# Optimization experiments

Hardware: AMD Instinct MI355X
Metric: run time of the kernel (lower is better)

Reference implementation:

```python
import jax, jax.numpy as jnp
import numpy as np

N = 50000      # nodes
E = 800000     # edges (avg degree 16)
IN = 256       # in_dim == heads*hidden (so DGL residual is Identity)
H = 4          # heads
D = 64         # hidden_dim / out_dim per head
EPS = 1e-5
NEG_SLOPE_ATTN = 0.2   # DGL GATConv edge-attention leaky_relu slope
NEG_SLOPE_ACT = 0.01   # F.leaky_relu default


def gat_conv(x, src, dst, W, al, ar, b, act):
    # x: [N, H*D], W: [H*D, H*D], al/ar: [H, D], b: [H*D]
    feat = (x @ W).reshape(N, H, D)                       # [N,H,D]
    el = jnp.sum(feat * al, axis=-1)                      # [N,H]
    er = jnp.sum(feat * ar, axis=-1)                      # [N,H]
    e = jax.nn.leaky_relu(el[src] + er[dst], NEG_SLOPE_ATTN)  # [E,H]
    # segment softmax over incoming edges per destination node
    m = jax.ops.segment_max(e, dst, num_segments=N)       # [N,H]
    m = jnp.where(jnp.isfinite(m), m, 0.0)                # nodes with no in-edges
    ee = jnp.exp(e - m[dst])                              # [E,H]
    denom = jax.ops.segment_sum(ee, dst, num_segments=N)  # [N,H]
    alpha = ee / jnp.maximum(denom[dst], 1e-9)            # [E,H]
    msg = feat[src] * alpha[:, :, None]                   # [E,H,D]
    rst = jax.ops.segment_sum(msg, dst, num_segments=N)   # [N,H,D]
    rst = rst + x.reshape(N, H, D)                        # identity residual (dims match)
    rst = rst + b.reshape(1, H, D)
    if act:
        rst = jax.nn.leaky_relu(rst, NEG_SLOPE_ACT)
    return rst


def batch_norm(h, gamma, beta):
    # BatchNorm1d in training mode: batch statistics over node dim
    mu = jnp.mean(h, axis=0)
    var = jnp.var(h, axis=0)
    return (h - mu) * jax.lax.rsqrt(var + EPS) * gamma + beta


def setup_inputs():
    key = jax.random.key(0)
    ks = jax.random.split(key, 18)
    s = 1.0 / np.sqrt(IN)
    inp = {
        'x': jax.random.normal(ks[0], (N, IN), jnp.float32),
        'src': jax.random.randint(ks[1], (E,), 0, N),
        'dst': jax.random.randint(ks[2], (E,), 0, N),
    }
    names = ['W1', 'al1', 'ar1', 'b1', 'W2', 'al2', 'ar2', 'b2', 'W3', 'al3', 'ar3', 'b3']
    shapes = [(IN, H * D), (H, D), (H, D), (H * D,)] * 3
    for i, (nm, sh) in enumerate(zip(names, shapes)):
        inp[nm] = jax.random.normal(ks[3 + i], sh, jnp.float32) * s
    inp['g1'] = jnp.ones((H * D,), jnp.float32)
    inp['be1'] = jnp.zeros((H * D,), jnp.float32)
    inp['g2'] = jnp.ones((H * D,), jnp.float32)
    inp['be2'] = jnp.zeros((H * D,), jnp.float32)
    return inp


def reference(x, src, dst, W1, al1, ar1, b1, W2, al2, ar2, b2, W3, al3, ar3, b3, g1, be1, g2, be2):
    h = gat_conv(x, src, dst, W1, al1, ar1, b1, act=True).reshape(N, H * D)
    h = batch_norm(h, g1, be1)
    h = gat_conv(h, src, dst, W2, al2, ar2, b2, act=True).reshape(N, H * D)
    h = batch_norm(h, g2, be2)
    h = gat_conv(h, src, dst, W3, al3, ar3, b3, act=False)   # [N,H,D]
    return h.mean(axis=1)                                    # [N,D]
```

## Files before the change

### kernel.cpp

```cpp
#include <hip/hip_runtime.h>

constexpr int NN = 50000;
constexpr int NE = 800000;
constexpr float SLOPE_A = 0.2f;
constexpr float SLOPE_R = 0.01f;
constexpr int SCB = 196;

typedef __attribute__((ext_vector_type(8))) short bf16x8;
typedef __attribute__((ext_vector_type(4))) float f32x4;

__device__ __forceinline__ unsigned short f2bf(float f) {
    union { float f; unsigned u; } v; v.f = f;
    unsigned u = v.u;
    unsigned r = u + 0x7fffu + ((u >> 16) & 1u);
    return (unsigned short)(r >> 16);
}
__device__ __forceinline__ float bf2f(unsigned short s) {
    union { unsigned u; float f; } v; v.u = ((unsigned)s) << 16;
    return v.f;
}

__global__ void k_hist(const int* __restrict__ dst, int* __restrict__ cnt) {
    int i = blockIdx.x * 256 + threadIdx.x;
    if (i < NE) atomicAdd(&cnt[dst[i]], 1);
}

__global__ void k_scan1(const int* __restrict__ cnt, int* __restrict__ loc,
                        int* __restrict__ bsum) {
    __shared__ int sh[256];
    int t = threadIdx.x;
    int i = blockIdx.x * 256 + t;
    int v = (i < NN) ? cnt[i] : 0;
    sh[t] = v;
    __syncthreads();
    for (int off = 1; off < 256; off <<= 1) {
        int tmp = (t >= off) ? sh[t - off] : 0;
        __syncthreads();
        sh[t] += tmp;
        __syncthreads();
    }
    loc[i] = sh[t] - v;
    if (t == 255) bsum[blockIdx.x] = sh[255];
}

__global__ void k_scan2(const int* __restrict__ bsum, int* __restrict__ boff,
                        int* __restrict__ rowptr) {
    __shared__ int sh[256];
    int t = threadIdx.x;
    int v = (t < SCB) ? bsum[t] : 0;
    sh[t] = v;
    __syncthreads();
    for (int off = 1; off < 256; off <<= 1) {
        int tmp = (t >= off) ? sh[t - off] : 0;
        __syncthreads();
        sh[t] += tmp;
        __syncthreads();
    }
    if (t < SCB) boff[t] = sh[t] - v;
    if (t == 255) rowptr[NN] = sh[255];
}

__global__ void k_scan3(const int* __restrict__ loc, const int* __restrict__ boff,
                        int* __restrict__ rowptr, int* __restrict__ cursor) {
    int i = blockIdx.x * 256 + threadIdx.x;
    if (i < NN) {
        int r = loc[i] + boff[blockIdx.x];
        rowptr[i] = r;
        cursor[i] = r;
    }
}

__global__ void k_scatter(const int* __restrict__ src, const int* __restrict__ dst,
                          int* __restrict__ cursor, int* __restrict__ ssrc) {
    int i = blockIdx.x * 256 + threadIdx.x;
    if (i < NE) {
        int d = dst[i];
        int pos = atomicAdd(&cursor[d], 1);
        ssrc[pos] = src[i];
    }
}

__global__ void k_fold(const float* __restrict__ W, const float* __restrict__ sc,
                       const float* __restrict__ sh, const float* __restrict__ al,
                       const float* __restrict__ ar, unsigned short* __restrict__ Wfrag,
                       float* __restrict__ cvec, unsigned short* __restrict__ wlrfrag,
                       float* __restrict__ offlr, int has_bn) {
    int b = blockIdx.x;
    if (b < 32) {
        int gid = b * 256 + threadIdx.x;
        int lane = gid & 63;
        int frag = gid >> 6;
        int j = frag & 3, kc = (frag >> 2) & 7, w = frag >> 5;
        int mm = lane & 15, q = lane >> 4;
        int n = 64 * w + 16 * j + mm;
        int k0 = kc * 32 + q * 8;
        unsigned short o[8];
#pragma unroll
        for (int t = 0; t < 8; t++) {
            float wv = W[(size_t)(k0 + t) * 256 + n];
            if (sc) wv *= sc[k0 + t];
            o[t] = f2bf(wv);
        }
        *(uint4*)(Wfrag + (size_t)gid * 8) = *(const uint4*)o;
    } else if (has_bn && b < 288) {
        __shared__ float red[256];
        int n = b - 32, k = threadIdx.x;
        red[k] = sh[k] * W[(size_t)k * 256 + n];
        __syncthreads();
        for (int off = 128; off > 0; off >>= 1) {
            if (k < off) red[k] += red[k + off];
            __syncthreads();
        }
        if (k == 0) cvec[n] = red[0];
    } else {
        int n = b - (has_bn ? 288 : 32);
        int h = n >> 1;
        const float* a = (n & 1) ? ar : al;
        int k = threadIdx.x;
        float raw = 0.f;
#pragma unroll 8
        for (int d = 0; d < 64; d++)
            raw += W[(size_t)k * 256 + 64 * h + d] * a[h * 64 + d];
        float val = (sc ? sc[k] : 1.f) * raw;
        int kc = k >> 5, rem = k & 31, q = rem >> 3, t = rem & 7;
        wlrfrag[kc * 512 + (q * 16 + n) * 8 + t] = f2bf(val);
        wlrfrag[kc * 512 + (q * 16 + n + 8) * 8 + t] = 0;
        __shared__ float red[256];
        red[k] = sh ? sh[k] * raw : 0.f;
        __syncthreads();
        for (int off = 128; off > 0; off >>= 1) {
            if (k < off) red[k] += red[k + off];
            __syncthreads();
        }
        if (k == 0) offlr[n] = red[0];
    }
}

__launch_bounds__(256)
__global__ void k_gemm(const void* __restrict__ Araw, int af32,
                       const unsigned short* __restrict__ Wfrag,
                       const float* __restrict__ cvec,
                       const unsigned short* __restrict__ wlrfrag,
                       const float* __restrict__ offlr,
                       unsigned short* __restrict__ feat16, float* __restrict__ el,
                       float* __restrict__ er) {
    constexpr int AP = 264;
    __shared__ __align__(16) unsigned short Alds[64 * AP];
    const int tid = threadIdx.x;
    const int rowbase = blockIdx.x * 64;

    if (af32) {
        const float* A = (const float*)Araw;
        int r = tid >> 6;
        int c4 = tid & 63;
        for (int it = 0; it < 16; it++) {
            int rr = it * 4 + r;
            int gr = rowbase + rr;
            float4 v = make_float4(0.f, 0.f, 0.f, 0.f);
            if (gr < NN) v = *(const float4*)(A + (size_t)gr * 256 + c4 * 4);
            ushort4 pv;
            pv.x = f2bf(v.x); pv.y = f2bf(v.y); pv.z = f2bf(v.z); pv.w = f2bf(v.w);
            *(ushort4*)(&Alds[rr * AP + c4 * 4]) = pv;
        }
    } else {
        const unsigned short* A = (const unsigned short*)Araw;
        for (int it = 0; it < 8; it++) {
            int idx = it * 256 + tid;
            int rr = idx >> 5;
            int c16 = idx & 31;
            int gr = rowbase + rr;
            uint4 v = make_uint4(0u, 0u, 0u, 0u);
            if (gr < NN) v = *(const uint4*)(A + (size_t)gr * 256 + c16 * 8);
            *(uint4*)(&Alds[rr * AP + c16 * 8]) = v;
        }
    }
    __syncthreads();

    f32x4 acc[4][4];
    for (int i = 0; i < 4; i++)
        for (int j = 0; j < 4; j++)
            acc[i][j] = (f32x4){0.f, 0.f, 0.f, 0.f};
    f32x4 accLR[4];
    for (int i = 0; i < 4; i++) accLR[i] = (f32x4){0.f, 0.f, 0.f, 0.f};

    const int lane = tid & 63, w = tid >> 6;
    const int mm = lane & 15, q = lane >> 4;

    const unsigned short* bbase = Wfrag + ((size_t)w * 8 * 4) * 512 + (size_t)lane * 8;

#pragma unroll
    for (int kc = 0; kc < 8; kc++) {
        bf16x8 a[4], b[4];
        for (int i = 0; i < 4; i++)
            a[i] = *(const bf16x8*)(&Alds[(16 * i + mm) * AP + kc * 32 + q * 8]);
        for (int j = 0; j < 4; j++)
            b[j] = *(const bf16x8*)(bbase + (size_t)(kc * 4 + j) * 512);
        for (int i = 0; i < 4; i++)
            for (int j = 0; j < 4; j++)
                acc[i][j] = __builtin_amdgcn_mfma_f32_16x16x32_bf16(a[i], b[j], acc[i][j], 0, 0, 0);
        if (w == 0) {
            bf16x8 blr = *(const bf16x8*)(wlrfrag + kc * 512 + lane * 8);
            for (int i = 0; i < 4; i++)
                accLR[i] = __builtin_amdgcn_mfma_f32_16x16x32_bf16(a[i], blr, accLR[i], 0, 0, 0);
        }
    }
    __syncthreads();

    if (cvec) {
        float cv[4];
        for (int j = 0; j < 4; j++) cv[j] = cvec[64 * w + 16 * j + mm];
        for (int i = 0; i < 4; i++)
            for (int j = 0; j < 4; j++)
                for (int r = 0; r < 4; r++)
                    acc[i][j][r] += cv[j];
    }

    if (w == 0 && mm < 8) {
        float off = offlr[mm];
        int h = mm >> 1;
        float* dstp = (mm & 1) ? er : el;
        for (int i = 0; i < 4; i++)
            for (int r = 0; r < 4; r++) {
                int gr = rowbase + 16 * i + q * 4 + r;
                if (gr < NN) dstp[gr * 4 + h] = accLR[i][r] + off;
            }
    }

    for (int i = 0; i < 4; i++)
        for (int j = 0; j < 4; j++) {
            int gc = 64 * w + 16 * j + mm;
            for (int r = 0; r < 4; r++) {
                int rr = 16 * i + q * 4 + r;
                Alds[rr * AP + gc] = f2bf(acc[i][j][r]);
            }
        }
    __syncthreads();
    for (int it = 0; it < 8; it++) {
        int idx = it * 256 + tid;
        int rr = idx >> 5;
        int c16 = idx & 31;
        int gr = rowbase + rr;
        if (gr < NN)
            *(uint4*)(feat16 + (size_t)gr * 256 + c16 * 8) = *(const uint4*)(&Alds[rr * AP + c16 * 8]);
    }
}

__launch_bounds__(256)
__global__ void k_agg(const unsigned short* __restrict__ feat16, const float* __restrict__ el,
                      const float* __restrict__ er, const int* __restrict__ rowptr,
                      const int* __restrict__ ssrc,
                      const unsigned short* __restrict__ residh, const float* __restrict__ residf,
                      const float* __restrict__ bnscale, const float* __restrict__ bnshift,
                      int use_bn, const float* __restrict__ bias, int act,
                      unsigned short* __restrict__ outh, float* __restrict__ outf,
                      int final_mean) {
    int n = __builtin_amdgcn_readfirstlane(blockIdx.x * 4 + (threadIdx.x >> 6));
    int l = threadIdx.x & 63;
    int h = l >> 4;
    int beg = rowptr[n], end = rowptr[n + 1];
    float erh = er[n * 4 + h];

    float4 r;
    if (residf) {
        r = *(const float4*)(residf + (size_t)n * 256 + l * 4);
    } else {
        ushort4 rv = *(const ushort4*)(residh + (size_t)n * 256 + l * 4);
        r = make_float4(bf2f(rv.x), bf2f(rv.y), bf2f(rv.z), bf2f(rv.w));
    }
    float4 sc4, sh4;
    if (use_bn) {
        sc4 = *(const float4*)(bnscale + l * 4);
        sh4 = *(const float4*)(bnshift + l * 4);
    }
    float4 bb = *(const float4*)(bias + l * 4);

    float d = 0.f;
    float4 acc = make_float4(0.f, 0.f, 0.f, 0.f);

    for (int e = beg; e < end; e += 8) {
        int ss[8];
        float cc[8];
        ushort4 ff[8];
#pragma unroll
        for (int j = 0; j < 8; j++) {
            int ee = e + j;
            ss[j] = ssrc[(ee < end) ? ee : beg];
        }
#pragma unroll
        for (int j = 0; j < 8; j++)
            cc[j] = el[ss[j] * 4 + h];
#pragma unroll
        for (int j = 0; j < 8; j++)
            ff[j] = *(const ushort4*)(feat16 + (size_t)ss[j] * 256 + l * 4);
#pragma unroll
        for (int j = 0; j < 8; j++) {
            float sc = cc[j] + erh;
            sc = (sc > 0.f) ? sc : SLOPE_A * sc;
            float wgt = ((e + j) < end) ? __expf(sc) : 0.f;
            d += wgt;
            acc.x += bf2f(ff[j].x) * wgt;
            acc.y += bf2f(ff[j].y) * wgt;
            acc.z += bf2f(ff[j].z) * wgt;
            acc.w += bf2f(ff[j].w) * wgt;
        }
    }

    float invd = 1.f / fmaxf(d, 1e-9f);
    acc.x *= invd; acc.y *= invd; acc.z *= invd; acc.w *= invd;

    if (use_bn) {
        r.x = r.x * sc4.x + sh4.x;
        r.y = r.y * sc4.y + sh4.y;
        r.z = r.z * sc4.z + sh4.z;
        r.w = r.w * sc4.w + sh4.w;
    }
    acc.x += r.x + bb.x; acc.y += r.y + bb.y;
    acc.z += r.z + bb.z; acc.w += r.w + bb.w;
    if (act) {
        acc.x = (acc.x > 0.f) ? acc.x : SLOPE_R * acc.x;
        acc.y = (acc.y > 0.f) ? acc.y : SLOPE_R * acc.y;
        acc.z = (acc.z > 0.f) ? acc.z : SLOPE_R * acc.z;
        acc.w = (acc.w > 0.f) ? acc.w : SLOPE_R * acc.w;
    }

    if (!final_mean) {
        ushort4 p;
        p.x = f2bf(acc.x); p.y = f2bf(acc.y); p.z = f2bf(acc.z); p.w = f2bf(acc.w);
        *(ushort4*)(outh + (size_t)n * 256 + l * 4) = p;
    } else {
        acc.x += __shfl_xor(acc.x, 16, 64); acc.x += __shfl_xor(acc.x, 32, 64);
        acc.y += __shfl_xor(acc.y, 16, 64); acc.y += __shfl_xor(acc.y, 32, 64);
        acc.z += __shfl_xor(acc.z, 16, 64); acc.z += __shfl_xor(acc.z, 32, 64);
        acc.w += __shfl_xor(acc.w, 16, 64); acc.w += __shfl_xor(acc.w, 32, 64);
        if (l < 16) {
            acc.x *= 0.25f; acc.y *= 0.25f; acc.z *= 0.25f; acc.w *= 0.25f;
            *(float4*)(outf + (size_t)n * 64 + l * 4) = acc;
        }
    }
}

__global__ void k_bnstats(const unsigned short* __restrict__ hh, float* __restrict__ pbuf) {
    __shared__ float ps[8 * 256];
    __shared__ float ps2[8 * 256];
    int t = threadIdx.x, b = blockIdx.x;
    int r8 = t >> 5, c32 = t & 31;
    int r0 = b * 196, r1 = min(r0 + 196, NN);
    float s[8], s2[8];
#pragma unroll
    for (int e = 0; e < 8; e++) { s[e] = 0.f; s2[e] = 0.f; }
    for (int r = r0 + r8; r < r1; r += 8) {
        uint4 v = *(const uint4*)(hh + (size_t)r * 256 + c32 * 8);
        const unsigned short* pv = (const unsigned short*)&v;
#pragma unroll
        for (int e = 0; e < 8; e++) {
            float f = bf2f(pv[e]);
            s[e] += f; s2[e] += f * f;
        }
    }
#pragma unroll
    for (int e = 0; e < 8; e++) {
        ps[r8 * 256 + c32 * 8 + e] = s[e];
        ps2[r8 * 256 + c32 * 8 + e] = s2[e];
    }
    __syncthreads();
    float ts = 0.f, ts2 = 0.f;
    for (int g = 0; g < 8; g++) { ts += ps[g * 256 + t]; ts2 += ps2[g * 256 + t]; }
    pbuf[b * 512 + t] = ts;
    pbuf[b * 512 + 256 + t] = ts2;
}

__global__ void k_bnfinal(const float* __restrict__ pbuf, const float* __restrict__ g,
                          const float* __restrict__ be, float* __restrict__ scale,
                          float* __restrict__ shift) {
    int t = threadIdx.x;
    float s = 0.f, s2 = 0.f;
    for (int b = 0; b < 256; b++) {
        s += pbuf[b * 512 + t];
        s2 += pbuf[b * 512 + 256 + t];
    }
    float mu = s * (1.f / NN);
    float var = s2 * (1.f / NN) - mu * mu;
    float rs = rsqrtf(var + 1e-5f);
    float sc = rs * g[t];
    scale[t] = sc;
    shift[t] = be[t] - mu * sc;
}

extern "C" void kernel_launch(void* const* d_in, const int* in_sizes, int n_in,
                              void* d_out, int out_size, void* d_ws, size_t ws_size,
                              hipStream_t stream) {
    const float* x   = (const float*)d_in[0];
    const int* src   = (const int*)d_in[1];
    const int* dst   = (const int*)d_in[2];
    const float* W1  = (const float*)d_in[3];
    const float* al1 = (const float*)d_in[4];
    const float* ar1 = (const float*)d_in[5];
    const float* b1  = (const float*)d_in[6];
    const float* W2  = (const float*)d_in[7];
    const float* al2 = (const float*)d_in[8];
    const float* ar2 = (const float*)d_in[9];
    const float* b2  = (const float*)d_in[10];
    const float* W3  = (const float*)d_in[11];
    const float* al3 = (const float*)d_in[12];
    const float* ar3 = (const float*)d_in[13];
    const float* b3  = (const float*)d_in[14];
    const float* g1  = (const float*)d_in[15];
    const float* be1 = (const float*)d_in[16];
    const float* g2  = (const float*)d_in[17];
    const float* be2 = (const float*)d_in[18];
    float* out = (float*)d_out;

    char* ws = (char*)d_ws;
    size_t off = 0;
    auto alloc = [&](size_t bytes) {
        void* p = ws + off;
        off += (bytes + 255) & ~(size_t)255;
        return p;
    };
    int* rowptr = (int*)alloc((NN + 1) * sizeof(int));
    int* cursor = (int*)alloc(NN * sizeof(int));
    int* cnt    = (int*)alloc(SCB * 256 * sizeof(int));
    int* loc    = (int*)alloc(SCB * 256 * sizeof(int));
    int* bsum   = (int*)alloc(SCB * sizeof(int));
    int* boff   = (int*)alloc(SCB * sizeof(int));
    int* ssrc   = (int*)alloc(NE * sizeof(int));
    unsigned short* feat16 = (unsigned short*)alloc((size_t)NN * 256 * sizeof(unsigned short));
    unsigned short* hbuf   = (unsigned short*)alloc((size_t)NN * 256 * sizeof(unsigned short));
    float* el   = (float*)alloc((size_t)NN * 4 * sizeof(float));
    float* er   = (float*)alloc((size_t)NN * 4 * sizeof(float));
    unsigned short* Wfrag1  = (unsigned short*)alloc(65536 * sizeof(unsigned short));
    unsigned short* Wfrag2  = (unsigned short*)alloc(65536 * sizeof(unsigned short));
    unsigned short* wlrfrag = (unsigned short*)alloc(4096 * sizeof(unsigned short));
    float* offlr   = (float*)alloc(16 * sizeof(float));
    float* cvec    = (float*)alloc(256 * sizeof(float));
    float* pbuf    = (float*)alloc(256 * 512 * sizeof(float));
    float* bnscale = (float*)alloc(256 * sizeof(float));
    float* bnshift = (float*)alloc(256 * sizeof(float));

    hipMemsetAsync(cnt, 0, NN * sizeof(int), stream);
    k_hist<<<(NE + 255) / 256, 256, 0, stream>>>(dst, cnt);
    k_scan1<<<SCB, 256, 0, stream>>>(cnt, loc, bsum);
    k_scan2<<<1, 256, 0, stream>>>(bsum, boff, rowptr);
    k_scan3<<<SCB, 256, 0, stream>>>(loc, boff, rowptr, cursor);
    k_scatter<<<(NE + 255) / 256, 256, 0, stream>>>(src, dst, cursor, ssrc);
    k_fold<<<40, 256, 0, stream>>>(W1, nullptr, nullptr, al1, ar1,
                                   Wfrag1, nullptr, wlrfrag, offlr, 0);

    const int GB = (NN + 63) / 64;
    const int NB = NN / 4;

    k_gemm<<<GB, 256, 0, stream>>>(x, 1, Wfrag1, nullptr, wlrfrag, offlr, feat16, el, er);
    k_agg<<<NB, 256, 0, stream>>>(feat16, el, er, rowptr, ssrc, nullptr, x,
                                  nullptr, nullptr, 0, b1, 1, hbuf, nullptr, 0);
    k_bnstats<<<256, 256, 0, stream>>>(hbuf, pbuf);
    k_bnfinal<<<1, 256, 0, stream>>>(pbuf, g1, be1, bnscale, bnshift);
    k_fold<<<296, 256, 0, stream>>>(W2, bnscale, bnshift, al2, ar2,
                                    Wfrag2, cvec, wlrfrag, offlr, 1);

    k_gemm<<<GB, 256, 0, stream>>>(hbuf, 0, Wfrag2, cvec, wlrfrag, offlr, feat16, el, er);
    k_agg<<<NB, 256, 0, stream>>>(feat16, el, er, rowptr, ssrc, hbuf, nullptr,
                                  bnscale, bnshift, 1, b2, 1, hbuf, nullptr, 0);
    k_bnstats<<<256, 256, 0, stream>>>(hbuf, pbuf);
    k_bnfinal<<<1, 256, 0, stream>>>(pbuf, g2, be2, bnscale, bnshift);
    k_fold<<<296, 256, 0, stream>>>(W3, bnscale, bnshift, al3, ar3,
                                    Wfrag2, cvec, wlrfrag, offlr, 1);

    k_gemm<<<GB, 256, 0, stream>>>(hbuf, 0, Wfrag2, cvec, wlrfrag, offlr, feat16, el, er);
    k_agg<<<NB, 256, 0, stream>>>(feat16, el, er, rowptr, ssrc, hbuf, nullptr,
                                  bnscale, bnshift, 1, b3, 0, nullptr, out, 1);
}
```

Measured before the change: 550.3 us.

## Precompute per-edge attention weights and split wave into two edge halves with 16-byte gathers

```diff
diff --git a/kernel.cpp b/kernel.cpp
--- a/kernel.cpp
+++ b/kernel.cpp
@@ -18,6 +18,12 @@
 __device__ __forceinline__ float bf2f(unsigned short s) {
     union { unsigned u; float f; } v; v.u = ((unsigned)s) << 16;
     return v.f;
+}
+__device__ __forceinline__ float bflo(unsigned u) {
+    union { unsigned u; float f; } v; v.u = u << 16; return v.f;
+}
+__device__ __forceinline__ float bfhi(unsigned u) {
+    union { unsigned u; float f; } v; v.u = u & 0xffff0000u; return v.f;
 }
 
 __global__ void k_hist(const int* __restrict__ dst, int* __restrict__ cnt) {
@@ -71,12 +77,14 @@
 }
 
 __global__ void k_scatter(const int* __restrict__ src, const int* __restrict__ dst,
-                          int* __restrict__ cursor, int* __restrict__ ssrc) {
+                          int* __restrict__ cursor, int* __restrict__ ssrc,
+                          int* __restrict__ sdst) {
     int i = blockIdx.x * 256 + threadIdx.x;
     if (i < NE) {
         int d = dst[i];
         int pos = atomicAdd(&cursor[d], 1);
         ssrc[pos] = src[i];
+        sdst[pos] = d;
     }
 }
 
@@ -245,10 +253,27 @@
     }
 }
 
+__global__ void k_wgt(const int* __restrict__ ssrc, const int* __restrict__ sdst,
+                      const float* __restrict__ el, const float* __restrict__ er,
+                      float* __restrict__ wgt) {
+    int pos = blockIdx.x * 256 + threadIdx.x;
+    if (pos >= NE) return;
+    int s = ssrc[pos], dd = sdst[pos];
+    float4 a = *(const float4*)(el + (size_t)s * 4);
+    float4 b = *(const float4*)(er + (size_t)dd * 4);
+    float4 o;
+    float v;
+    v = a.x + b.x; v = (v > 0.f) ? v : SLOPE_A * v; o.x = __expf(v);
+    v = a.y + b.y; v = (v > 0.f) ? v : SLOPE_A * v; o.y = __expf(v);
+    v = a.z + b.z; v = (v > 0.f) ? v : SLOPE_A * v; o.z = __expf(v);
+    v = a.w + b.w; v = (v > 0.f) ? v : SLOPE_A * v; o.w = __expf(v);
+    *(float4*)(wgt + (size_t)pos * 4) = o;
+}
+
 __launch_bounds__(256)
-__global__ void k_agg(const unsigned short* __restrict__ feat16, const float* __restrict__ el,
-                      const float* __restrict__ er, const int* __restrict__ rowptr,
-                      const int* __restrict__ ssrc,
+__global__ void k_agg(const unsigned short* __restrict__ feat16,
+                      const float* __restrict__ wgt,
+                      const int* __restrict__ rowptr, const int* __restrict__ ssrc,
                       const unsigned short* __restrict__ residh, const float* __restrict__ residf,
                       const float* __restrict__ bnscale, const float* __restrict__ bnshift,
                       int use_bn, const float* __restrict__ bias, int act,
@@ -256,85 +281,108 @@
                       int final_mean) {
     int n = __builtin_amdgcn_readfirstlane(blockIdx.x * 4 + (threadIdx.x >> 6));
     int l = threadIdx.x & 63;
-    int h = l >> 4;
+    int p = l >> 5;
+    int q = l & 31;
+    int c8 = q * 8;
+    int hh = q >> 3;
     int beg = rowptr[n], end = rowptr[n + 1];
-    float erh = er[n * 4 + h];
-
-    float4 r;
+
+    float r[8];
     if (residf) {
-        r = *(const float4*)(residf + (size_t)n * 256 + l * 4);
+        float4 r0 = *(const float4*)(residf + (size_t)n * 256 + c8);
+        float4 r1 = *(const float4*)(residf + (size_t)n * 256 + c8 + 4);
+        r[0] = r0.x; r[1] = r0.y; r[2] = r0.z; r[3] = r0.w;
+        r[4] = r1.x; r[5] = r1.y; r[6] = r1.z; r[7] = r1.w;
     } else {
-        ushort4 rv = *(const ushort4*)(residh + (size_t)n * 256 + l * 4);
-        r = make_float4(bf2f(rv.x), bf2f(rv.y), bf2f(rv.z), bf2f(rv.w));
-    }
-    float4 sc4, sh4;
+        uint4 rv = *(const uint4*)(residh + (size_t)n * 256 + c8);
+        r[0] = bflo(rv.x); r[1] = bfhi(rv.x);
+        r[2] = bflo(rv.y); r[3] = bfhi(rv.y);
+        r[4] = bflo(rv.z); r[5] = bfhi(rv.z);
+        r[6] = bflo(rv.w); r[7] = bfhi(rv.w);
+    }
+
+    float d = 0.f;
+    float acc[8];
+#pragma unroll
+    for (int k = 0; k < 8; k++) acc[k] = 0.f;
+
+    for (int e = beg; e < end; e += 8) {
+        int ss[4];
+        float ww[4];
+        uint4 ff[4];
+#pragma unroll
+        for (int s = 0; s < 4; s++) {
+            int idx = e + 2 * s + p;
+            int cidx = (idx < end) ? idx : beg;
+            ss[s] = ssrc[cidx];
+            float wv = wgt[(size_t)cidx * 4 + hh];
+            ww[s] = (idx < end) ? wv : 0.f;
+        }
+#pragma unroll
+        for (int s = 0; s < 4; s++)
+            ff[s] = *(const uint4*)(feat16 + (size_t)ss[s] * 256 + c8);
+#pragma unroll
+        for (int s = 0; s < 4; s++) {
+            float w = ww[s];
+            d += w;
+            acc[0] += bflo(ff[s].x) * w; acc[1] += bfhi(ff[s].x) * w;
+            acc[2] += bflo(ff[s].y) * w; acc[3] += bfhi(ff[s].y) * w;
+            acc[4] += bflo(ff[s].z) * w; acc[5] += bfhi(ff[s].z) * w;
+            acc[6] += bflo(ff[s].w) * w; acc[7] += bfhi(ff[s].w) * w;
+        }
+    }
+
+    d += __shfl_xor(d, 32, 64);
+#pragma unroll
+    for (int k = 0; k < 8; k++) acc[k] += __shfl_xor(acc[k], 32, 64);
+
+    float invd = 1.f / fmaxf(d, 1e-9f);
+#pragma unroll
+    for (int k = 0; k < 8; k++) acc[k] *= invd;
+
     if (use_bn) {
-        sc4 = *(const float4*)(bnscale + l * 4);
-        sh4 = *(const float4*)(bnshift + l * 4);
-    }
-    float4 bb = *(const float4*)(bias + l * 4);
-
-    float d = 0.f;
-    float4 acc = make_float4(0.f, 0.f, 0.f, 0.f);
-
-    for (int e = beg; e < end; e += 8) {
-        int ss[8];
-        float cc[8];
-        ushort4 ff[8];
-#pragma unroll
-        for (int j = 0; j < 8; j++) {
-            int ee = e + j;
-            ss[j] = ssrc[(ee < end) ? ee : beg];
-        }
-#pragma unroll
-        for (int j = 0; j < 8; j++)
-            cc[j] = el[ss[j] * 4 + h];
-#pragma unroll
-        for (int j = 0; j < 8; j++)
-            ff[j] = *(const ushort4*)(feat16 + (size_t)ss[j] * 256 + l * 4);
-#pragma unroll
-        for (int j = 0; j < 8; j++) {
-            float sc = cc[j] + erh;
-            sc = (sc > 0.f) ? sc : SLOPE_A * sc;
-            float wgt = ((e + j) < end) ? __expf(sc) : 0.f;
-            d += wgt;
-            acc.x += bf2f(ff[j].x) * wgt;
-            acc.y += bf2f(ff[j].y) * wgt;
-            acc.z += bf2f(ff[j].z) * wgt;
-            acc.w += bf2f(ff[j].w) * wgt;
-        }
-    }
-
-    float invd = 1.f / fmaxf(d, 1e-9f);
-    acc.x *= invd; acc.y *= invd; acc.z *= invd; acc.w *= invd;
-
-    if (use_bn) {
-        r.x = r.x * sc4.x + sh4.x;
-        r.y = r.y * sc4.y + sh4.y;
-        r.z = r.z * sc4.z + sh4.z;
-        r.w = r.w * sc4.w + sh4.w;
-    }
-    acc.x += r.x + bb.x; acc.y += r.y + bb.y;
-    acc.z += r.z + bb.z; acc.w += r.w + bb.w;
+        float4 s0 = *(const float4*)(bnscale + c8);
+        float4 s1 = *(const float4*)(bnscale + c8 + 4);
+        float4 h0 = *(const float4*)(bnshift + c8);
+        float4 h1 = *(const float4*)(bnshift + c8 + 4);
+        r[0] = r[0] * s0.x + h0.x; r[1] = r[1] * s0.y + h0.y;
+        r[2] = r[2] * s0.z + h0.z; r[3] = r[3] * s0.w + h0.w;
+        r[4] = r[4] * s1.x + h1.x; r[5] = r[5] * s1.y + h1.y;
+        r[6] = r[6] * s1.z + h1.z; r[7] = r[7] * s1.w + h1.w;
+    }
+    {
+        float4 b0 = *(const float4*)(bias + c8);
+        float4 b1 = *(const float4*)(bias + c8 + 4);
+        acc[0] += r[0] + b0.x; acc[1] += r[1] + b0.y;
+        acc[2] += r[2] + b0.z; acc[3] += r[3] + b0.w;
+        acc[4] += r[4] + b1.x; acc[5] += r[5] + b1.y;
+        acc[6] += r[6] + b1.z; acc[7] += r[7] + b1.w;
+    }
     if (act) {
-        acc.x = (acc.x > 0.f) ? acc.x : SLOPE_R * acc.x;
-        acc.y = (acc.y > 0.f) ? acc.y : SLOPE_R * acc.y;
-        acc.z = (acc.z > 0.f) ? acc.z : SLOPE_R * acc.z;
-        acc.w = (acc.w > 0.f) ? acc.w : SLOPE_R * acc.w;
+#pragma unroll
+        for (int k = 0; k < 8; k++) acc[k] = (acc[k] > 0.f) ? acc[k] : SLOPE_R * acc[k];
     }
 
     if (!final_mean) {
-        ushort4 p;
-        p.x = f2bf(acc.x); p.y = f2bf(acc.y); p.z = f2bf(acc.z); p.w = f2bf(acc.w);
-        *(ushort4*)(outh + (size_t)n * 256 + l * 4) = p;
+        if (p == 0) {
+            uint4 o;
+            o.x = (unsigned)f2bf(acc[0]) | ((unsigned)f2bf(acc[1]) << 16);
+            o.y = (unsigned)f2bf(acc[2]) | ((unsigned)f2bf(acc[3]) << 16);
+            o.z = (unsigned)f2bf(acc[4]) | ((unsigned)f2bf(acc[5]) << 16);
+            o.w = (unsigned)f2bf(acc[6]) | ((unsigned)f2bf(acc[7]) << 16);
+            *(uint4*)(outh + (size_t)n * 256 + c8) = o;
+        }
     } else {
-        acc.x += __shfl_xor(acc.x, 16, 64); acc.x += __shfl_xor(acc.x, 32, 64);
-        acc.y += __shfl_xor(acc.y, 16, 64); acc.y += __shfl_xor(acc.y, 32, 64);
-        acc.z += __shfl_xor(acc.z, 16, 64); acc.z += __shfl_xor(acc.z, 32, 64);
-        acc.w += __shfl_xor(acc.w, 16, 64); acc.w += __shfl_xor(acc.w, 32, 64);
-        if (l < 16) {
-            acc.x *= 0.25f; acc.y *= 0.25f; acc.z *= 0.25f; acc.w *= 0.25f;
-            *(float4*)(outf + (size_t)n * 64 + l * 4) = acc;
+#pragma unroll
+        for (int k = 0; k < 8; k++) {
+            acc[k] += __shfl_xor(acc[k], 8, 64);
+            acc[k] += __shfl_xor(acc[k], 16, 64);
+        }
+        if (p == 0 && q < 8) {
+            float4 o0 = make_float4(acc[0] * 0.25f, acc[1] * 0.25f, acc[2] * 0.25f, acc[3] * 0.25f);
+            float4 o1 = make_float4(acc[4] * 0.25f, acc[5] * 0.25f, acc[6] * 0.25f, acc[7] * 0.25f);
+            *(float4*)(outf + (size_t)n * 64 + c8) = o0;
+            *(float4*)(outf + (size_t)n * 64 + c8 + 4) = o1;
         }
     }
 }
@@ -424,6 +472,8 @@
     int* bsum   = (int*)alloc(SCB * sizeof(int));
     int* boff   = (int*)alloc(SCB * sizeof(int));
     int* ssrc   = (int*)alloc(NE * sizeof(int));
+    int* sdst   = (int*)alloc(NE * sizeof(int));
+    float* wgt  = (float*)alloc((size_t)NE * 4 * sizeof(float));
     unsigned short* feat16 = (unsigned short*)alloc((size_t)NN * 256 * sizeof(unsigned short));
     unsigned short* hbuf   = (unsigned short*)alloc((size_t)NN * 256 * sizeof(unsigned short));
     float* el   = (float*)alloc((size_t)NN * 4 * sizeof(float));
@@ -442,15 +492,17 @@
     k_scan1<<<SCB, 256, 0, stream>>>(cnt, loc, bsum);
     k_scan2<<<1, 256, 0, stream>>>(bsum, boff, rowptr);
     k_scan3<<<SCB, 256, 0, stream>>>(loc, boff, rowptr, cursor);
-    k_scatter<<<(NE + 255) / 256, 256, 0, stream>>>(src, dst, cursor, ssrc);
+    k_scatter<<<(NE + 255) / 256, 256, 0, stream>>>(src, dst, cursor, ssrc, sdst);
     k_fold<<<40, 256, 0, stream>>>(W1, nullptr, nullptr, al1, ar1,
                                    Wfrag1, nullptr, wlrfrag, offlr, 0);
 
     const int GB = (NN + 63) / 64;
     const int NB = NN / 4;
+    const int EB = (NE + 255) / 256;
 
     k_gemm<<<GB, 256, 0, stream>>>(x, 1, Wfrag1, nullptr, wlrfrag, offlr, feat16, el, er);
-    k_agg<<<NB, 256, 0, stream>>>(feat16, el, er, rowptr, ssrc, nullptr, x,
+    k_wgt<<<EB, 256, 0, stream>>>(ssrc, sdst, el, er, wgt);
+    k_agg<<<NB, 256, 0, stream>>>(feat16, wgt, rowptr, ssrc, nullptr, x,
                                   nullptr, nullptr, 0, b1, 1, hbuf, nullptr, 0);
     k_bnstats<<<256, 256, 0, stream>>>(hbuf, pbuf);
     k_bnfinal<<<1, 256, 0, stream>>>(pbuf, g1, be1, bnscale, bnshift);
@@ -458,7 +510,8 @@
                                     Wfrag2, cvec, wlrfrag, offlr, 1);
 
     k_gemm<<<GB, 256, 0, stream>>>(hbuf, 0, Wfrag2, cvec, wlrfrag, offlr, feat16, el, er);
-    k_agg<<<NB, 256, 0, stream>>>(feat16, el, er, rowptr, ssrc, hbuf, nullptr,
+    k_wgt<<<EB, 256, 0, stream>>>(ssrc, sdst, el, er, wgt);
+    k_agg<<<NB, 256, 0, stream>>>(feat16, wgt, rowptr, ssrc, hbuf, nullptr,
                                   bnscale, bnshift, 1, b2, 1, hbuf, nullptr, 0);
     k_bnstats<<<256, 256, 0, stream>>>(hbuf, pbuf);
     k_bnfinal<<<1, 256, 0, stream>>>(pbuf, g2, be2, bnscale, bnshift);
@@ -466,6 +519,7 @@
                                     Wfrag2, cvec, wlrfrag, offlr, 1);
 
     k_gemm<<<GB, 256, 0, stream>>>(hbuf, 0, Wfrag2, cvec, wlrfrag, offlr, feat16, el, er);
-    k_agg<<<NB, 256, 0, stream>>>(feat16, el, er, rowptr, ssrc, hbuf, nullptr,
+    k_wgt<<<EB, 256, 0, stream>>>(ssrc, sdst, el, er, wgt);
+    k_agg<<<NB, 256, 0, stream>>>(feat16, wgt, rowptr, ssrc, hbuf, nullptr,
                                   bnscale, bnshift, 1, b3, 0, nullptr, out, 1);
 }
```

New measurement: 558.7 us. About the same (+1.5%).
